# Kernel optimization log

Measured on AMD Instinct MI355X. Metric: run time of the kernel, lower is better.

The kernel has to match this reference:

```python
import jax, jax.numpy as jnp
import numpy as np

N_LAYERS = 6
D_MODEL = 272          # num_variables
D_STATE = 64           # d_state
D_INNER = 2 * D_MODEL  # expand=2 -> 544
D_CONV = 4
DT_RANK = 17           # ceil(272/16)
N_SCORES = 4
B, L = 4, 2048


def setup_inputs():
    key = jax.random.key(0)
    ks = jax.random.split(key, 10)
    def rn(k, shape, s=0.02):
        return jax.random.normal(k, shape, dtype=jnp.float32) * s
    A_init = jnp.broadcast_to(jnp.arange(1, D_STATE + 1, dtype=jnp.float32), (N_LAYERS, D_INNER, D_STATE))
    return {
        "x": jax.random.normal(ks[0], (B, L, D_MODEL), dtype=jnp.float32),
        "ln_w": jnp.ones((N_LAYERS, D_MODEL), jnp.float32),
        "ln_b": jnp.zeros((N_LAYERS, D_MODEL), jnp.float32),
        "in_proj_w": rn(ks[1], (N_LAYERS, 2 * D_INNER, D_MODEL)),
        "conv_w": rn(ks[2], (N_LAYERS, D_INNER, D_CONV), 0.2),
        "conv_b": jnp.zeros((N_LAYERS, D_INNER), jnp.float32),
        "x_proj_w": rn(ks[3], (N_LAYERS, DT_RANK + 2 * D_STATE, D_INNER)),
        "dt_proj_w": rn(ks[4], (N_LAYERS, D_INNER, DT_RANK), 0.1),
        "dt_proj_b": rn(ks[5], (N_LAYERS, D_INNER), 0.5),
        "A_log": jnp.log(A_init),
        "Dskip": jnp.ones((N_LAYERS, D_INNER), jnp.float32),
        "out_proj_w": rn(ks[6], (N_LAYERS, D_MODEL, D_INNER)),
        "reg_w": rn(ks[7], (N_SCORES, D_MODEL)),
        "reg_b": jnp.zeros((N_SCORES,), jnp.float32),
    }


def _layernorm(x, w, b, eps=1e-5):
    mu = x.mean(-1, keepdims=True)
    var = ((x - mu) ** 2).mean(-1, keepdims=True)
    return (x - mu) * jax.lax.rsqrt(var + eps) * w + b


def _selective_scan(u, delta, A, Bm, C, Dd):
    # u, delta: (b,l,d); Bm, C: (b,l,n); A: (d,n); Dd: (d,)
    def step(h, inp):
        d_t, B_t, C_t, u_t = inp                           # (b,d),(b,n),(b,n),(b,d)
        dA = jnp.exp(d_t[:, :, None] * A)                  # (b,d,n)
        h = dA * h + (d_t * u_t)[:, :, None] * B_t[:, None, :]
        return h, jnp.einsum('bdn,bn->bd', h, C_t)
    h0 = jnp.zeros((u.shape[0], A.shape[0], A.shape[1]), u.dtype)
    xs = tuple(jnp.swapaxes(a, 0, 1) for a in (delta, Bm, C, u))  # time-major
    _, ys = jax.lax.scan(step, h0, xs)
    return jnp.swapaxes(ys, 0, 1) + u * Dd


def _mamba_block(x, ln_w, ln_b, Wi, cw, cb, Wx, Wdt, bdt, A_log, Dd, Wo):
    h = _layernorm(x, ln_w, ln_b)
    xi, z = jnp.split(h @ Wi.T, 2, axis=-1)                # (b,l,d_inner) each
    xp = jnp.pad(xi, ((0, 0), (D_CONV - 1, 0), (0, 0)))    # causal depthwise conv
    xc = sum(xp[:, k:k + xi.shape[1], :] * cw[:, k] for k in range(D_CONV)) + cb
    xc = jax.nn.silu(xc)
    dbl = xc @ Wx.T                                        # (b,l,dt_rank+2n)
    dt, Bm, C = jnp.split(dbl, [DT_RANK, DT_RANK + D_STATE], axis=-1)
    delta = jax.nn.softplus(dt @ Wdt.T + bdt)
    y = _selective_scan(xc, delta, -jnp.exp(A_log), Bm, C, Dd)
    y = y * jax.nn.silu(z)
    return x + y @ Wo.T                                    # residual


def reference(x, ln_w, ln_b, in_proj_w, conv_w, conv_b, x_proj_w, dt_proj_w, dt_proj_b, A_log, Dskip, out_proj_w, reg_w, reg_b):
    for i in range(N_LAYERS):
        x = _mamba_block(x, ln_w[i], ln_b[i], in_proj_w[i], conv_w[i], conv_b[i],
                         x_proj_w[i], dt_proj_w[i], dt_proj_b[i], A_log[i], Dskip[i], out_proj_w[i])
    feat = x.mean(axis=1)                                  # (b, d_model)
    scores = feat @ reg_w.T + reg_b                        # (b, n_scores)
    return (scores, feat)
```

## Files before the change

kernel.cpp:

```cpp
#include <hip/hip_runtime.h>
#include <hip/hip_bf16.h>
#include <math.h>

#define NL 6
#define DM 272
#define DS 64
#define DI 544
#define DTR 17
#define NSC 4
#define BB 4
#define LL 2048
#define MTOK (BB*LL)
#define TCH 128
#define CH  16
#define DQ  (DI/4)

typedef __attribute__((ext_vector_type(8))) short bf16x8;
typedef __attribute__((ext_vector_type(4))) float f32x4;

__device__ __forceinline__ float sigmoidf_(float x){ return 1.0f/(1.0f+__expf(-x)); }
__device__ __forceinline__ unsigned short f2bfu(float x){
    union { __hip_bfloat16 h; unsigned short u; } c; c.h = __float2bfloat16(x); return c.u;
}
__device__ __forceinline__ float bfu2f(unsigned short u){ return __uint_as_float(((unsigned)u)<<16); }
__device__ __forceinline__ float exp2x(float x){ float r; asm("v_exp_f32 %0, %1" : "=v"(r) : "v"(x)); return r; }

#define DPPADD(x, ctrl) x += __int_as_float(__builtin_amdgcn_update_dpp(0, __float_as_int(x), ctrl, 0xf, 0xf, true))
__device__ __forceinline__ float wsum64(float x){
    DPPADD(x, 0x111); DPPADD(x, 0x112); DPPADD(x, 0x114); DPPADD(x, 0x118);
    DPPADD(x, 0x142); DPPADD(x, 0x143);
    return x;
}

__global__ __launch_bounds__(256) void ln_kernel(const float* __restrict__ X,
                          const float* __restrict__ w,
                          const float* __restrict__ b,
                          unsigned short* __restrict__ Hb)
{
    int wave = threadIdx.x >> 6;
    int lane = threadIdx.x & 63;
    int tok = blockIdx.x*4 + wave;
    const float* xr = X + (size_t)tok*DM;
    float v[5];
    float s=0.f, ss=0.f;
    #pragma unroll
    for (int j=0;j<5;++j){
        int idx = lane + j*64;
        float x = (idx < DM) ? xr[idx] : 0.f;
        v[j]=x; s+=x; ss+=x*x;
    }
    #pragma unroll
    for (int off=1; off<64; off<<=1){ s += __shfl_xor(s,off); ss += __shfl_xor(ss,off); }
    float mu  = s * (1.0f/DM);
    float var = ss*(1.0f/DM) - mu*mu;
    float inv = 1.0f/sqrtf(var + 1e-5f);
    unsigned short* hr = Hb + (size_t)tok*DM;
    #pragma unroll
    for (int j=0;j<5;++j){
        int idx = lane + j*64;
        if (idx<DM) hr[idx] = f2bfu((v[j]-mu)*inv*w[idx] + b[idx]);
    }
}

template<bool RESID, bool OUTBF16>
__global__ __launch_bounds__(256) void gmfma(const unsigned short* __restrict__ A, int lda,
                     const unsigned short* __restrict__ W, int ldw,
                     void* __restrict__ Cv, int ldc,
                     const float* __restrict__ R, int ldr,
                     int N, int K)
{
    __shared__ unsigned short As[128*40];
    __shared__ unsigned short Bs[128*40];
    int bm = blockIdx.x*128, bn = blockIdx.y*128;
    int tid = threadIdx.x;
    int lane = tid & 63, wave = tid >> 6;
    int wm = wave >> 1, wn = wave & 1;
    f32x4 acc[4][4] = {};
    int r16 = lane & 15, kg = (lane >> 4) * 8;
    for (int k0=0; k0<K; k0+=32){
        #pragma unroll
        for (int it=0; it<2; ++it){
            int cid = tid + it*256;
            int row = cid >> 2, kq = (cid & 3)*8;
            int kk = k0 + kq;
            uint4 za = make_uint4(0,0,0,0);
            if (kk < K) za = *(const uint4*)(A + (size_t)(bm+row)*lda + kk);
            *(uint4*)&As[row*40 + kq] = za;
            uint4 zb = make_uint4(0,0,0,0);
            int wr = bn + row;
            if (wr < N && kk < K) zb = *(const uint4*)(W + (size_t)wr*ldw + kk);
            *(uint4*)&Bs[row*40 + kq] = zb;
        }
        __syncthreads();
        bf16x8 af[4], bfr[4];
        #pragma unroll
        for (int mi=0; mi<4; ++mi)
            af[mi] = *(bf16x8*)&As[(wm*64 + mi*16 + r16)*40 + kg];
        #pragma unroll
        for (int ni=0; ni<4; ++ni)
            bfr[ni] = *(bf16x8*)&Bs[(wn*64 + ni*16 + r16)*40 + kg];
        #pragma unroll
        for (int mi=0; mi<4; ++mi)
            #pragma unroll
            for (int ni=0; ni<4; ++ni)
                acc[mi][ni] = __builtin_amdgcn_mfma_f32_16x16x32_bf16(af[mi], bfr[ni], acc[mi][ni], 0, 0, 0);
        __syncthreads();
    }
    int rowt = (lane >> 4)*4, colt = lane & 15;
    #pragma unroll
    for (int mi=0; mi<4; ++mi){
        #pragma unroll
        for (int ni=0; ni<4; ++ni){
            int col = bn + wn*64 + ni*16 + colt;
            if (col < N){
                #pragma unroll
                for (int j=0; j<4; ++j){
                    int row = bm + wm*64 + mi*16 + rowt + j;
                    float v = acc[mi][ni][j];
                    if (RESID) v += R[(size_t)row*ldr + col];
                    if (OUTBF16)
                        ((unsigned short*)Cv)[(size_t)row*ldc + col] = f2bfu(v);
                    else
                        ((float*)Cv)[(size_t)row*ldc + col] = v;
                }
            }
        }
    }
}

__global__ __launch_bounds__(256) void conv_t2_kernel(const unsigned short* __restrict__ XZb,
                                 const float* __restrict__ cw,
                                 const float* __restrict__ cb,
                                 unsigned short* __restrict__ XCtb,
                                 unsigned short* __restrict__ Gtb,
                                 unsigned short* __restrict__ XCb)
{
    __shared__ float xi[67][69];
    __shared__ float zz[64][69];
    int bid = blockIdx.x;
    int b  = bid >> 8;
    int rem = bid & 255;
    int t0 = (rem >> 3)*64;
    int d0 = (rem & 7)*68;
    int tid = threadIdx.x;
    for (int li = tid; li < 67*17; li += 256){
        int row = li / 17, q = li - row*17;
        int tg = t0 - 3 + row;
        float4 v = make_float4(0.f,0.f,0.f,0.f);
        if (tg >= 0){
            ushort4 u4 = *(const ushort4*)(XZb + ((size_t)b*LL + tg)*(2*DI) + d0 + q*4);
            v.x = bfu2f(u4.x); v.y = bfu2f(u4.y); v.z = bfu2f(u4.z); v.w = bfu2f(u4.w);
        }
        xi[row][q*4+0]=v.x; xi[row][q*4+1]=v.y; xi[row][q*4+2]=v.z; xi[row][q*4+3]=v.w;
    }
    for (int li = tid; li < 64*17; li += 256){
        int row = li / 17, q = li - row*17;
        ushort4 u4 = *(const ushort4*)(XZb + ((size_t)b*LL + t0 + row)*(2*DI) + DI + d0 + q*4);
        zz[row][q*4+0]=bfu2f(u4.x); zz[row][q*4+1]=bfu2f(u4.y);
        zz[row][q*4+2]=bfu2f(u4.z); zz[row][q*4+3]=bfu2f(u4.w);
    }
    __syncthreads();
    int t = tid & 63;
    int dw = tid >> 6;
    float xcreg[17];
    #pragma unroll
    for (int i=0; i<17; ++i){
        int dl = dw + i*4;
        int d = d0 + dl;
        const float* cwd = cw + d*4;
        float acc = cb[d];
        #pragma unroll
        for (int k=0;k<4;++k) acc = fmaf(xi[t+k][dl], cwd[k], acc);
        float xc = acc * sigmoidf_(acc);
        float z  = zz[t][dl];
        size_t o = ((size_t)b*DI + d)*LL + t0 + t;
        XCtb[o] = f2bfu(xc);
        Gtb[o]  = f2bfu(z * sigmoidf_(z));
        xcreg[i] = xc;
    }
    __syncthreads();
    #pragma unroll
    for (int i=0; i<17; ++i) zz[t][dw + i*4] = xcreg[i];
    __syncthreads();
    for (int li = tid; li < 64*17; li += 256){
        int row = li / 17, q = li - row*17;
        ushort4 v;
        v.x = f2bfu(zz[row][q*4+0]); v.y = f2bfu(zz[row][q*4+1]);
        v.z = f2bfu(zz[row][q*4+2]); v.w = f2bfu(zz[row][q*4+3]);
        *(ushort4*)&XCb[((size_t)b*LL + t0 + row)*DI + d0 + q*4] = v;
    }
}

__global__ __launch_bounds__(256) void dt_t2_kernel(const float* __restrict__ DBLb,
                          const float* __restrict__ Wdt,
                          const float* __restrict__ bdt,
                          float* __restrict__ DELt)
{
    __shared__ float dtv[64*19];
    __shared__ float wl[68*17];
    int bid = blockIdx.x;
    int b  = bid >> 8;
    int rem = bid & 255;
    int t0 = (rem >> 3)*64;
    int d0 = (rem & 7)*68;
    int tid = threadIdx.x;
    for (int li = tid; li < 64*17; li += 256){
        int row = li / 17, col = li - row*17;
        dtv[row*19 + col] = DBLb[((size_t)b*LL + t0 + row)*145 + col];
    }
    for (int li = tid; li < 68*17; li += 256)
        wl[li] = Wdt[(size_t)d0*17 + li];
    __syncthreads();
    int t = tid & 63;
    #pragma unroll 1
    for (int dl = tid >> 6; dl < 68; dl += 4){
        float s = bdt[d0 + dl];
        #pragma unroll
        for (int r=0;r<DTR;++r) s = fmaf(dtv[t*19 + r], wl[dl*17 + r], s);
        float sp = (s > 20.f) ? s : log1pf(__expf(s));
        DELt[((size_t)b*DI + d0 + dl)*LL + t0 + t] = sp;
    }
}

__global__ __launch_bounds__(256) void scan_a(const float* __restrict__ DELt,
                       const unsigned short* __restrict__ XCtb,
                       const float* __restrict__ DBLb,
                       const float* __restrict__ A_log,
                       float* __restrict__ Q,
                       float* __restrict__ S)
{
    __shared__ float2 dlb[4][4][64];
    int wave = threadIdx.x >> 6, lane = threadIdx.x & 63;
    float2 (*Db)[64] = dlb[wave];
    int wid = blockIdx.x*4 + wave;
    int dd = wid % DQ;
    int c  = (wid / DQ) % CH;
    int b  = wid / (DQ*CH);
    int d0 = dd, d1 = dd+DQ, d2 = dd+2*DQ, d3 = dd+3*DQ;
    const float L2E = 1.44269504f;
    float Av0 = -__expf(A_log[d0*DS + lane]) * L2E;
    float Av1 = -__expf(A_log[d1*DS + lane]) * L2E;
    float Av2 = -__expf(A_log[d2*DS + lane]) * L2E;
    float Av3 = -__expf(A_log[d3*DS + lane]) * L2E;
    float h0=0.f,h1=0.f,h2=0.f,h3=0.f, ds0=0.f,ds1=0.f,ds2=0.f,ds3=0.f;
    size_t rb0 = ((size_t)b*DI + d0)*LL + c*TCH;
    size_t rb1 = ((size_t)b*DI + d1)*LL + c*TCH;
    size_t rb2 = ((size_t)b*DI + d2)*LL + c*TCH;
    size_t rb3 = ((size_t)b*DI + d3)*LL + c*TCH;
    const float* pB = DBLb + ((size_t)b*LL + c*TCH)*145;
    for (int blk=0; blk<TCH/64; ++blk){
        size_t o0 = rb0 + blk*64 + lane, o1 = rb1 + blk*64 + lane;
        size_t o2 = rb2 + blk*64 + lane, o3 = rb3 + blk*64 + lane;
        float dl0 = DELt[o0], dl1 = DELt[o1], dl2 = DELt[o2], dl3 = DELt[o3];
        float du0 = dl0*bfu2f(XCtb[o0]), du1 = dl1*bfu2f(XCtb[o1]);
        float du2 = dl2*bfu2f(XCtb[o2]), du3 = dl3*bfu2f(XCtb[o3]);
        ds0 += dl0; ds1 += dl1; ds2 += dl2; ds3 += dl3;
        Db[0][lane] = make_float2(dl0, du0);
        Db[1][lane] = make_float2(dl1, du1);
        Db[2][lane] = make_float2(dl2, du2);
        Db[3][lane] = make_float2(dl3, du3);
        const float* p = pB + (size_t)blk*64*145;
        #pragma unroll 1
        for (int g=0; g<8; ++g){
            const float2* q0 = &Db[0][g*8];
            const float2* q1 = &Db[1][g*8];
            const float2* q2 = &Db[2][g*8];
            const float2* q3 = &Db[3][g*8];
            #pragma unroll
            for (int i=0; i<8; ++i){
                float Bv = p[17+lane];
                float2 a0=q0[i], a1=q1[i], a2=q2[i], a3=q3[i];
                h0 = fmaf(exp2x(a0.x*Av0), h0, a0.y*Bv);
                h1 = fmaf(exp2x(a1.x*Av1), h1, a1.y*Bv);
                h2 = fmaf(exp2x(a2.x*Av2), h2, a2.y*Bv);
                h3 = fmaf(exp2x(a3.x*Av3), h3, a3.y*Bv);
                p += 145;
            }
        }
    }
    size_t q0i = ((size_t)b*DI + d0)*CH + c, q1i = ((size_t)b*DI + d1)*CH + c;
    size_t q2i = ((size_t)b*DI + d2)*CH + c, q3i = ((size_t)b*DI + d3)*CH + c;
    Q[q0i*64 + lane] = h0; Q[q1i*64 + lane] = h1;
    Q[q2i*64 + lane] = h2; Q[q3i*64 + lane] = h3;
    float s0 = wsum64(ds0), s1 = wsum64(ds1), s2 = wsum64(ds2), s3 = wsum64(ds3);
    if (lane == 63){ S[q0i]=s0; S[q1i]=s1; S[q2i]=s2; S[q3i]=s3; }
}

__global__ __launch_bounds__(256) void scan_c(const float* __restrict__ DELt,
                       const unsigned short* __restrict__ XCtb,
                       const unsigned short* __restrict__ Gtb,
                       const float* __restrict__ DBLb,
                       const float* __restrict__ A_log,
                       const float* __restrict__ Dskip,
                       const float* __restrict__ Q,
                       const float* __restrict__ S,
                       unsigned short* __restrict__ Yb)
{
    __shared__ float P[4][2][4][76];
    __shared__ float Ypark[4][2][4];
    __shared__ float2 dlb[4][2][64];
    int wave = threadIdx.x >> 6, lane = threadIdx.x & 63;
    float (*Pr0)[76] = P[wave][0];
    float (*Pr1)[76] = P[wave][1];
    float* Yp0 = Ypark[wave][0];
    float* Yp1 = Ypark[wave][1];
    float2* Db0 = dlb[wave][0];
    float2* Db1 = dlb[wave][1];
    int wid = blockIdx.x*4 + wave;
    int dd = wid % (DI/2);
    int c  = (wid / (DI/2)) % CH;
    int b  = wid / ((DI/2)*CH);
    int d0 = dd, d1 = dd + DI/2;
    const float L2E = 1.44269504f;
    float Av0 = -__expf(A_log[d0*DS + lane]) * L2E;
    float Av1 = -__expf(A_log[d1*DS + lane]) * L2E;
    float Dd0 = Dskip[d0], Dd1 = Dskip[d1];
    size_t q0 = ((size_t)b*DI + d0)*CH, q1 = ((size_t)b*DI + d1)*CH;
    float h0=0.f, h1=0.f;
    for (int j=0; j<c; ++j){
        h0 = fmaf(exp2x(Av0*S[q0+j]), h0, Q[(q0+j)*64 + lane]);
        h1 = fmaf(exp2x(Av1*S[q1+j]), h1, Q[(q1+j)*64 + lane]);
    }
    size_t rb0 = ((size_t)b*DI + d0)*LL + c*TCH;
    size_t rb1 = ((size_t)b*DI + d1)*LL + c*TCH;
    const float* pB = DBLb + ((size_t)b*LL + c*TCH)*145;
    int fr = lane >> 4, fq = (lane & 15)*4;
    for (int blk=0; blk<TCH/64; ++blk){
        size_t o0 = rb0 + blk*64 + lane, o1 = rb1 + blk*64 + lane;
        float dl0 = DELt[o0], dl1 = DELt[o1];
        float ul0 = bfu2f(XCtb[o0]), ul1 = bfu2f(XCtb[o1]);
        float gl0 = bfu2f(Gtb[o0]),  gl1 = bfu2f(Gtb[o1]);
        Db0[lane] = make_float2(dl0, dl0*ul0);
        Db1[lane] = make_float2(dl1, dl1*ul1);
        float y0=0.f, y1=0.f;
        const float* p = pB + (size_t)blk*64*145;
        #pragma unroll 1
        for (int f=0; f<16; ++f){
            const float2* db0 = &Db0[f*4];
            const float2* db1 = &Db1[f*4];
            #pragma unroll
            for (int i=0; i<4; ++i){
                float Bv = p[17+lane];
                float Cv = p[81+lane];
                float2 a0 = db0[i], a1 = db1[i];
                h0 = fmaf(exp2x(a0.x*Av0), h0, a0.y*Bv);
                h1 = fmaf(exp2x(a1.x*Av1), h1, a1.y*Bv);
                Pr0[i][lane] = h0*Cv;
                Pr1[i][lane] = h1*Cv;
                p += 145;
            }
            float4 xa0 = *(const float4*)&Pr0[fr][fq];
            float s0 = (xa0.x+xa0.y)+(xa0.z+xa0.w);
            DPPADD(s0,0x111); DPPADD(s0,0x112); DPPADD(s0,0x114); DPPADD(s0,0x118);
            float4 xa1 = *(const float4*)&Pr1[fr][fq];
            float s1 = (xa1.x+xa1.y)+(xa1.z+xa1.w);
            DPPADD(s1,0x111); DPPADD(s1,0x112); DPPADD(s1,0x114); DPPADD(s1,0x118);
            if ((lane & 15) == 15){ Yp0[fr] = s0; Yp1[fr] = s1; }
            float g0 = Yp0[lane & 3];
            float g1 = Yp1[lane & 3];
            if ((lane >> 2) == f){ y0 = g0; y1 = g1; }
        }
        size_t trow = (size_t)b*LL + c*TCH + blk*64 + lane;
        Yb[trow*DI + d0] = f2bfu((y0 + ul0*Dd0)*gl0);
        Yb[trow*DI + d1] = f2bfu((y1 + ul1*Dd1)*gl1);
    }
}

__global__ __launch_bounds__(256) void wconv_kernel(const float* __restrict__ src,
                            unsigned short* __restrict__ dst,
                            int total, int kin, int kout)
{
    int idx = blockIdx.x*256 + threadIdx.x;
    if (idx >= total) return;
    int r = idx / kout, c = idx - r*kout;
    float v = (c < kin) ? src[(size_t)r*kin + c] : 0.f;
    dst[idx] = f2bfu(v);
}

__global__ __launch_bounds__(256) void head1_kernel(const float* __restrict__ X,
                             float* __restrict__ Pt)
{
    int b = blockIdx.x >> 6, c = blockIdx.x & 63;
    int tid = threadIdx.x;
    for (int dm = tid; dm < DM; dm += 256){
        float s = 0.f;
        const float* base = X + ((size_t)b*LL + c*32)*DM + dm;
        #pragma unroll 8
        for (int tt=0; tt<32; ++tt) s += base[(size_t)tt*DM];
        Pt[(size_t)(b*64 + c)*DM + dm] = s;
    }
}

__global__ __launch_bounds__(256) void head2_kernel(const float* __restrict__ Pt,
                             const float* __restrict__ reg_w,
                             const float* __restrict__ reg_b,
                             float* __restrict__ out)
{
    __shared__ float feat[DM];
    int b = blockIdx.x, tid = threadIdx.x;
    for (int dm = tid; dm < DM; dm += 256){
        float s = 0.f;
        for (int c=0; c<64; ++c) s += Pt[(size_t)(b*64 + c)*DM + dm];
        float f = s * (1.0f/LL);
        feat[dm] = f;
        out[16 + b*DM + dm] = f;
    }
    __syncthreads();
    if (tid < NSC){
        float s = reg_b[tid];
        const float* wr = reg_w + tid*DM;
        for (int k=0;k<DM;++k) s = fmaf(feat[k], wr[k], s);
        out[b*NSC + tid] = s;
    }
}

extern "C" void kernel_launch(void* const* d_in, const int* in_sizes, int n_in,
                              void* d_out, int out_size, void* d_ws, size_t ws_size,
                              hipStream_t stream)
{
    const float* x_in  = (const float*)d_in[0];
    const float* ln_w  = (const float*)d_in[1];
    const float* ln_b  = (const float*)d_in[2];
    const float* Wi    = (const float*)d_in[3];
    const float* cw    = (const float*)d_in[4];
    const float* cb    = (const float*)d_in[5];
    const float* Wx    = (const float*)d_in[6];
    const float* Wdt   = (const float*)d_in[7];
    const float* bdt   = (const float*)d_in[8];
    const float* A_log = (const float*)d_in[9];
    const float* Dd    = (const float*)d_in[10];
    const float* Wo    = (const float*)d_in[11];
    const float* regw  = (const float*)d_in[12];
    const float* regb  = (const float*)d_in[13];
    float* out = (float*)d_out;

    char* base = (char*)d_ws;
    auto carve = [&](size_t bytes) -> char* {
        char* p = base; base += (bytes + 255) & ~(size_t)255; return p;
    };
    unsigned short* XZb  = (unsigned short*)carve((size_t)MTOK*1088*2);
    unsigned short* XCtb = (unsigned short*)carve((size_t)MTOK*544*2);
    unsigned short* Gtb  = (unsigned short*)carve((size_t)MTOK*544*2);
    float*          DELt = (float*)carve((size_t)MTOK*544*4);
    float*          DBLb = (float*)carve((size_t)MTOK*145*4);
    float*          Xb   = (float*)carve((size_t)MTOK*272*4);
    unsigned short* Yb   = (unsigned short*)carve((size_t)MTOK*544*2);
    char*           SCR  = carve((size_t)MTOK*272*4);
    float*          Sbuf = (float*)carve((size_t)BB*DI*CH*4);
    unsigned short* WiB  = (unsigned short*)carve((size_t)NL*1088*DM*2);
    unsigned short* WxB  = (unsigned short*)carve((size_t)NL*145*DI*2);
    unsigned short* WoB  = (unsigned short*)carve((size_t)NL*272*DI*2);

    unsigned short* Hb  = (unsigned short*)SCR;
    unsigned short* XCb = (unsigned short*)SCR;
    float*          Q   = (float*)SCR;
    float*          Pt  = (float*)SCR;

    (void)hipMemcpyAsync(Xb, x_in, sizeof(float)*(size_t)MTOK*DM, hipMemcpyDeviceToDevice, stream);

    wconv_kernel<<<(NL*1088*DM + 255)/256, 256, 0, stream>>>(Wi, WiB, NL*1088*DM, DM, DM);
    wconv_kernel<<<(NL*145*DI + 255)/256, 256, 0, stream>>>(Wx, WxB, NL*145*DI, DI, DI);
    wconv_kernel<<<(NL*272*DI + 255)/256, 256, 0, stream>>>(Wo, WoB, NL*272*DI, DI, DI);

    for (int l=0; l<NL; ++l){
        ln_kernel<<<MTOK/4, 256, 0, stream>>>(Xb, ln_w + l*DM, ln_b + l*DM, Hb);
        gmfma<false,true><<<dim3(MTOK/128, (2*DI+127)/128), 256, 0, stream>>>(
            Hb, DM, WiB + (size_t)l*2*DI*DM, DM, XZb, 2*DI, nullptr, 0, 2*DI, DM);
        conv_t2_kernel<<<BB*256, 256, 0, stream>>>(XZb, cw + l*DI*4, cb + l*DI, XCtb, Gtb, XCb);
        gmfma<false,false><<<dim3(MTOK/128, 2), 256, 0, stream>>>(
            XCb, DI, WxB + (size_t)l*145*DI, DI, DBLb, 145, nullptr, 0, 145, DI);
        dt_t2_kernel<<<BB*256, 256, 0, stream>>>(DBLb, Wdt + (size_t)l*DI*DTR, bdt + l*DI, DELt);
        scan_a<<<(BB*CH*DQ)/4, 256, 0, stream>>>(DELt, XCtb, DBLb,
                                                 A_log + (size_t)l*DI*DS, Q, Sbuf);
        scan_c<<<(BB*CH*(DI/2))/4, 256, 0, stream>>>(DELt, XCtb, Gtb, DBLb,
                                                     A_log + (size_t)l*DI*DS, Dd + l*DI, Q, Sbuf, Yb);
        gmfma<true,false><<<dim3(MTOK/128, 3), 256, 0, stream>>>(
            Yb, DI, WoB + (size_t)l*DM*DI, DI, Xb, DM, Xb, DM, DM, DI);
    }
    head1_kernel<<<BB*64, 256, 0, stream>>>(Xb, Pt);
    head2_kernel<<<BB, 256, 0, stream>>>(Pt, regw, regb, out);
}
```

Measured before the change: 1.543 ms.

## Stage scan B-vectors in shared memory and coalesce Y stores via LDS

In scan_a, the block cooperatively loads the 64x64 B slice for each 64-step sub-block into shared memory and register-prefetches the next sub-block, replacing per-wave strided global reads of B. In scan_c, the four waves' bf16 outputs are gathered in a small LDS tile and written back as 8-byte vector stores instead of scattered 2-byte stores. This is meant to cut redundant global loads and uncoalesced writes, at the cost of extra block-wide barriers and more LDS and register use. The scan_c path assumes that all four waves of a block share the same batch and chunk and cover four consecutive d indices.

```diff
diff --git a/kernel.cpp b/kernel.cpp
--- a/kernel.cpp
+++ b/kernel.cpp
@@ -230,7 +230,9 @@
                        float* __restrict__ S)
 {
     __shared__ float2 dlb[4][4][64];
-    int wave = threadIdx.x >> 6, lane = threadIdx.x & 63;
+    __shared__ float Bsh[64][68];
+    int tid = threadIdx.x;
+    int wave = tid >> 6, lane = tid & 63;
     float2 (*Db)[64] = dlb[wave];
     int wid = blockIdx.x*4 + wave;
     int dd = wid % DQ;
@@ -247,8 +249,29 @@
     size_t rb1 = ((size_t)b*DI + d1)*LL + c*TCH;
     size_t rb2 = ((size_t)b*DI + d2)*LL + c*TCH;
     size_t rb3 = ((size_t)b*DI + d3)*LL + c*TCH;
-    const float* pB = DBLb + ((size_t)b*LL + c*TCH)*145;
+    const float* pBB = DBLb + ((size_t)b*LL + (size_t)c*TCH)*145;
+    float rg[16];
+    #pragma unroll
+    for (int k=0;k<16;++k){
+        int li = tid + k*256;
+        rg[k] = pBB[(size_t)(li>>6)*145 + 17 + (li&63)];
+    }
     for (int blk=0; blk<TCH/64; ++blk){
+        __syncthreads();
+        #pragma unroll
+        for (int k=0;k<16;++k){
+            int li = tid + k*256;
+            Bsh[li>>6][li&63] = rg[k];
+        }
+        __syncthreads();
+        if (blk+1 < TCH/64){
+            const float* nb = pBB + (size_t)(blk+1)*64*145;
+            #pragma unroll
+            for (int k=0;k<16;++k){
+                int li = tid + k*256;
+                rg[k] = nb[(size_t)(li>>6)*145 + 17 + (li&63)];
+            }
+        }
         size_t o0 = rb0 + blk*64 + lane, o1 = rb1 + blk*64 + lane;
         size_t o2 = rb2 + blk*64 + lane, o3 = rb3 + blk*64 + lane;
         float dl0 = DELt[o0], dl1 = DELt[o1], dl2 = DELt[o2], dl3 = DELt[o3];
@@ -259,7 +282,6 @@
         Db[1][lane] = make_float2(dl1, du1);
         Db[2][lane] = make_float2(dl2, du2);
         Db[3][lane] = make_float2(dl3, du3);
-        const float* p = pB + (size_t)blk*64*145;
         #pragma unroll 1
         for (int g=0; g<8; ++g){
             const float2* q0 = &Db[0][g*8];
@@ -268,13 +290,12 @@
             const float2* q3 = &Db[3][g*8];
             #pragma unroll
             for (int i=0; i<8; ++i){
-                float Bv = p[17+lane];
+                float Bv = Bsh[g*8+i][lane];
                 float2 a0=q0[i], a1=q1[i], a2=q2[i], a3=q3[i];
                 h0 = fmaf(exp2x(a0.x*Av0), h0, a0.y*Bv);
                 h1 = fmaf(exp2x(a1.x*Av1), h1, a1.y*Bv);
                 h2 = fmaf(exp2x(a2.x*Av2), h2, a2.y*Bv);
                 h3 = fmaf(exp2x(a3.x*Av3), h3, a3.y*Bv);
-                p += 145;
             }
         }
     }
@@ -299,7 +320,9 @@
     __shared__ float P[4][2][4][76];
     __shared__ float Ypark[4][2][4];
     __shared__ float2 dlb[4][2][64];
-    int wave = threadIdx.x >> 6, lane = threadIdx.x & 63;
+    __shared__ unsigned short Yst[64][12];
+    int tid = threadIdx.x;
+    int wave = tid >> 6, lane = tid & 63;
     float (*Pr0)[76] = P[wave][0];
     float (*Pr1)[76] = P[wave][1];
     float* Yp0 = Ypark[wave][0];
@@ -311,6 +334,10 @@
     int c  = (wid / (DI/2)) % CH;
     int b  = wid / ((DI/2)*CH);
     int d0 = dd, d1 = dd + DI/2;
+    int wid0 = blockIdx.x*4;
+    int dd0b = wid0 % (DI/2);
+    int cB = (wid0 / (DI/2)) % CH;
+    int bB = wid0 / ((DI/2)*CH);
     const float L2E = 1.44269504f;
     float Av0 = -__expf(A_log[d0*DS + lane]) * L2E;
     float Av1 = -__expf(A_log[d1*DS + lane]) * L2E;
@@ -360,9 +387,16 @@
             float g1 = Yp1[lane & 3];
             if ((lane >> 2) == f){ y0 = g0; y1 = g1; }
         }
-        size_t trow = (size_t)b*LL + c*TCH + blk*64 + lane;
-        Yb[trow*DI + d0] = f2bfu((y0 + ul0*Dd0)*gl0);
-        Yb[trow*DI + d1] = f2bfu((y1 + ul1*Dd1)*gl1);
+        Yst[lane][wave]     = f2bfu((y0 + ul0*Dd0)*gl0);
+        Yst[lane][4 + wave] = f2bfu((y1 + ul1*Dd1)*gl1);
+        __syncthreads();
+        if (tid < 128){
+            int row = tid & 63, grp = tid >> 6;
+            ushort4 v = *(const ushort4*)&Yst[row][grp*4];
+            size_t trow = (size_t)bB*LL + (size_t)cB*TCH + blk*64 + row;
+            *(ushort4*)&Yb[trow*DI + dd0b + grp*(DI/2)] = v;
+        }
+        __syncthreads();
     }
 }
 
```

Result: slower. 1.587 ms (+2.8%).
